# Kernel optimization log

Measured on AMD Instinct MI355X. Metric: run time of the kernel, lower is better.

The kernel has to match this reference:

```python
import jax, jax.numpy as jnp
import numpy as np

N_NODES = 20000
N_EDGES = 320000
N_GRAPHS = 64
F_IN = 128
HID = 128
K = 3
LEAK = 0.01  # nn.LeakyReLU default negative_slope


def _glorot(key, shape):
    fan_in, fan_out = shape[-2], shape[-1]
    s = jnp.sqrt(2.0 / (fan_in + fan_out))
    return jax.random.normal(key, shape, dtype=jnp.float32) * s


def setup_inputs() -> dict:
    key = jax.random.key(0)
    ks = jax.random.split(key, 12)
    x = jax.random.normal(ks[0], (N_NODES, F_IN), dtype=jnp.float32)
    edge_index = jax.random.randint(ks[1], (2, N_EDGES), 0, N_NODES, dtype=jnp.int64)
    batch = jnp.sort(jax.random.randint(ks[2], (N_NODES,), 0, N_GRAPHS, dtype=jnp.int64))
    # K-hop GraphConv weights: (K+1) matrices per layer
    W1 = _glorot(ks[3], (K + 1, F_IN, HID));       b1 = jnp.zeros((HID,), jnp.float32)
    W2 = _glorot(ks[4], (K + 1, HID, 2 * HID));    b2 = jnp.zeros((2 * HID,), jnp.float32)
    W3 = _glorot(ks[5], (K + 1, 2 * HID, 4 * HID)); b3 = jnp.zeros((4 * HID,), jnp.float32)
    # classifier MLP
    Wm1 = _glorot(ks[6], (4 * HID, 1024)); bm1 = jnp.zeros((1024,), jnp.float32)
    Wm2 = _glorot(ks[7], (1024, 512));     bm2 = jnp.zeros((512,), jnp.float32)
    Wm3 = _glorot(ks[8], (512, 4));        bm3 = jnp.zeros((4,), jnp.float32)
    return dict(x=x, edge_index=edge_index, batch=batch,
                W1=W1, b1=b1, W2=W2, b2=b2, W3=W3, b3=b3,
                Wm1=Wm1, bm1=bm1, Wm2=Wm2, bm2=bm2, Wm3=Wm3, bm3=bm3)


def _khop_conv(x, src, dst, W, b):
    # out = sum_{k=0..K} (A^k x) W_k + b, A = scatter-sum of src features onto dst
    h = x
    out = h @ W[0]
    for k in range(1, W.shape[0]):
        h = jax.ops.segment_sum(h[src], dst, num_segments=N_NODES)  # one hop
        out = out + h @ W[k]
    return out + b


def reference(x, edge_index, batch, W1, b1, W2, b2, W3, b3, Wm1, bm1, Wm2, bm2, Wm3, bm3):
    src, dst = edge_index[0], edge_index[1]
    h = _khop_conv(x, src, dst, W1, b1)
    h = jnp.where(h > 0, h, LEAK * h)
    h = _khop_conv(h, src, dst, W2, b2)
    h = jnp.where(h > 0, h, LEAK * h)
    h = _khop_conv(h, src, dst, W3, b3)
    # global max pool per graph -> [N_GRAPHS, 4*HID]
    g = jax.ops.segment_max(h, batch, num_segments=N_GRAPHS)
    # classifier head
    g = jax.nn.relu(g @ Wm1 + bm1)
    g = jax.nn.relu(g @ Wm2 + bm2)
    return g @ Wm3 + bm3
```

## Files before the change

kernel.cpp:

```cpp
#include <hip/hip_runtime.h>
#include <stdint.h>

#define NN 20000
#define NNP 20096
#define NE 320000
#define NG 64

typedef unsigned short u16;
typedef __attribute__((ext_vector_type(8))) short short8;
typedef __attribute__((ext_vector_type(4))) float f32x4;

__device__ __forceinline__ void glds16(const void* g, const void* l) {
    __builtin_amdgcn_global_load_lds((const __attribute__((address_space(1))) void*)g,
                                     (__attribute__((address_space(3))) void*)l, 16, 0, 0);
}

__device__ __forceinline__ u16 f2bf(float f) {
    unsigned u = __float_as_uint(f);
    return (u16)((u + 0x7FFFu + ((u >> 16) & 1u)) >> 16);
}

__global__ void hist_kernel(const int* __restrict__ dst, int* __restrict__ cnt, int E) {
    int i = blockIdx.x * blockDim.x + threadIdx.x;
    if (i < E) atomicAdd(&cnt[dst[i]], 1);
}

__global__ void scan_kernel(const int* __restrict__ cnt, int* __restrict__ rp, int n) {
    __shared__ int part[1024];
    int tid = threadIdx.x;
    const int CH = (n + 1023) / 1024;
    int base = tid * CH;
    int s = 0;
    for (int i = 0; i < CH; i++) { int idx = base + i; if (idx < n) s += cnt[idx]; }
    part[tid] = s;
    __syncthreads();
    for (int off = 1; off < 1024; off <<= 1) {
        int v = (tid >= off) ? part[tid - off] : 0;
        __syncthreads();
        part[tid] += v;
        __syncthreads();
    }
    int run = (tid == 0) ? 0 : part[tid - 1];
    for (int i = 0; i < CH; i++) {
        int idx = base + i;
        if (idx < n) { rp[idx] = run; run += cnt[idx]; }
    }
    if (tid == 1023) rp[n] = part[1023];
}

__global__ void copy_int(const int* __restrict__ a, int* __restrict__ b, int n) {
    int i = blockIdx.x * blockDim.x + threadIdx.x;
    if (i < n) b[i] = a[i];
}

__global__ void scatter_kernel(const int* __restrict__ src, const int* __restrict__ dstv,
                               int* __restrict__ ofs, int* __restrict__ col, int E) {
    int i = blockIdx.x * blockDim.x + threadIdx.x;
    if (i < E) {
        int p = atomicAdd(&ofs[dstv[i]], 1);
        col[p] = src[i];
    }
}

__global__ void conv_x(const float* __restrict__ x, u16* __restrict__ S1) {
    int i = blockIdx.x * blockDim.x + threadIdx.x;
    if (i >= NN * 128 / 8) return;
    int row = i >> 4, c = (i & 15) * 8;
    const float* p = x + (size_t)row * 128 + c;
    uint4 r;
    unsigned* pr = (unsigned*)&r;
#pragma unroll
    for (int j = 0; j < 4; j++)
        pr[j] = (unsigned)f2bf(p[2 * j]) | ((unsigned)f2bf(p[2 * j + 1]) << 16);
    *(uint4*)(S1 + (size_t)row * 512 + c) = r;
}

__global__ void convT(const float* __restrict__ W, u16* __restrict__ WT, int K, int M) {
    __shared__ float tile[32][33];
    int m0 = blockIdx.x * 32, k0 = blockIdx.y * 32;
    int tx = threadIdx.x & 31, ty = threadIdx.x >> 5;
#pragma unroll
    for (int i = 0; i < 32; i += 8)
        tile[ty + i][tx] = W[(size_t)(k0 + ty + i) * M + m0 + tx];
    __syncthreads();
#pragma unroll
    for (int i = 0; i < 32; i += 8)
        WT[(size_t)(m0 + ty + i) * K + k0 + tx] = f2bf(tile[tx][ty + i]);
}

__global__ void g2bf(const unsigned* __restrict__ genc, u16* __restrict__ gb) {
    int i = blockIdx.x * blockDim.x + threadIdx.x;
    if (i >= NG * 512) return;
    unsigned u = genc[i];
    u = (u & 0x80000000u) ? (u ^ 0x80000000u) : ~u;
    gb[i] = f2bf(__uint_as_float(u));
}

template <int NCHUNK>
__global__ __launch_bounds__(256) void prop_bf16(
    const int* __restrict__ rp, const int* __restrict__ col,
    u16* __restrict__ S, int stride, int in_off, int out_off) {
    constexpr int NPB = 256 / NCHUNK;
    int node = blockIdx.x * NPB + (threadIdx.x / NCHUNK);
    int c = threadIdx.x & (NCHUNK - 1);
    if (node >= NN) return;
    int s0 = rp[node], s1 = rp[node + 1];
    float acc[8] = {};
    const u16* base = S + in_off + c * 8;
    auto accum = [&](uint4 v) {
        const unsigned* pv = (const unsigned*)&v;
#pragma unroll
        for (int j = 0; j < 4; j++) {
            acc[2 * j]     += __uint_as_float(pv[j] << 16);
            acc[2 * j + 1] += __uint_as_float(pv[j] & 0xFFFF0000u);
        }
    };
    int e = s0;
    for (; e + 4 <= s1; e += 4) {
        int i0 = col[e], i1 = col[e + 1], i2 = col[e + 2], i3 = col[e + 3];
        uint4 v0 = *(const uint4*)(base + (size_t)i0 * stride);
        uint4 v1 = *(const uint4*)(base + (size_t)i1 * stride);
        uint4 v2 = *(const uint4*)(base + (size_t)i2 * stride);
        uint4 v3 = *(const uint4*)(base + (size_t)i3 * stride);
        accum(v0); accum(v1); accum(v2); accum(v3);
    }
    for (; e < s1; e++)
        accum(*(const uint4*)(base + (size_t)col[e] * stride));
    uint4 r;
    unsigned* pr = (unsigned*)&r;
#pragma unroll
    for (int j = 0; j < 4; j++)
        pr[j] = (unsigned)f2bf(acc[2 * j]) | ((unsigned)f2bf(acc[2 * j + 1]) << 16);
    *(uint4*)(S + (size_t)node * stride + out_off + c * 8) = r;
}

template <int TM, int EPI, int ACT>
__global__ __launch_bounds__(256) void gemm_bf16(
    const u16* __restrict__ A, int lda, const u16* __restrict__ BT,
    int Kp, int M, const float* __restrict__ bias,
    u16* __restrict__ outB, int ldo,
    unsigned* __restrict__ genc, const int* __restrict__ batch) {
    __shared__ u16 Al[TM * 32];
    __shared__ u16 Bl[128 * 32];
    __shared__ unsigned gbuf[EPI == 1 ? 256 : 4];
    constexpr int MR = TM / 32;
    int col0 = blockIdx.x * 128, row0 = blockIdx.y * TM;
    int t = threadIdx.x;
    int w = t >> 6, ln = t & 63;
    int wm = (w >> 1) * (TM / 2), wn = (w & 1) * 64;
    int srowB = w * 32 + (ln >> 2);
    int srowA = (TM == 128) ? srowB : (w * 16 + (ln >> 2));
    int skc = (ln & 3) * 8;
    f32x4 acc[MR][4] = {};

    if (EPI == 1) gbuf[t] = 0;

    for (int k0 = 0; k0 < Kp; k0 += 32) {
        if (TM == 128) {
            glds16(A + (size_t)(row0 + srowA) * lda + k0 + skc,      &Al[w * 1024]);
            glds16(A + (size_t)(row0 + srowA + 16) * lda + k0 + skc, &Al[w * 1024 + 512]);
        } else {
            glds16(A + (size_t)(row0 + srowA) * lda + k0 + skc,      &Al[w * 512]);
        }
        glds16(BT + (size_t)(col0 + srowB) * Kp + k0 + skc,          &Bl[w * 1024]);
        glds16(BT + (size_t)(col0 + srowB + 16) * Kp + k0 + skc,     &Bl[w * 1024 + 512]);
        __syncthreads();
        short8 af[MR], bf[4];
#pragma unroll
        for (int m = 0; m < MR; m++)
            af[m] = *(const short8*)&Al[(wm + m * 16 + (ln & 15)) * 32 + (ln >> 4) * 8];
#pragma unroll
        for (int n = 0; n < 4; n++)
            bf[n] = *(const short8*)&Bl[(wn + n * 16 + (ln & 15)) * 32 + (ln >> 4) * 8];
#pragma unroll
        for (int m = 0; m < MR; m++)
#pragma unroll
            for (int n = 0; n < 4; n++)
                acc[m][n] = __builtin_amdgcn_mfma_f32_16x16x32_bf16(af[m], bf[n], acc[m][n], 0, 0, 0);
        __syncthreads();
    }

    int g_lo = (EPI == 1) ? batch[row0] : 0;
#pragma unroll
    for (int m = 0; m < MR; m++) {
#pragma unroll
        for (int r = 0; r < 4; r++) {
            int row = row0 + wm + m * 16 + (ln >> 4) * 4 + r;
            if (row < NN) {
                int gb_ = 0, gidx = 0;
                if (EPI == 1) { gb_ = batch[row]; gidx = gb_ - g_lo; }
#pragma unroll
                for (int n = 0; n < 4; n++) {
                    int cl = wn + n * 16 + (ln & 15);
                    float v = acc[m][n][r] + bias[col0 + cl];
                    if (EPI == 0) {
                        v = ACT ? fmaxf(v, 0.f) : (v > 0.f ? v : 0.01f * v);
                        outB[(size_t)row * ldo + col0 + cl] = f2bf(v);
                    } else {
                        unsigned u = __float_as_uint(v);
                        u = (u & 0x80000000u) ? ~u : (u | 0x80000000u);
                        if (gidx < 2) atomicMax(&gbuf[gidx * 128 + cl], u);
                        else          atomicMax(&genc[(size_t)gb_ * M + col0 + cl], u);
                    }
                }
            }
        }
    }
    if (EPI == 1) {
        __syncthreads();
        int j = t >> 7, c = t & 127;
        unsigned u = gbuf[j * 128 + c];
        if (u && g_lo + j < NG) atomicMax(&genc[(size_t)(g_lo + j) * M + col0 + c], u);
    }
}

__global__ void head3(const u16* __restrict__ m2b, const float* __restrict__ W,
                      const float* __restrict__ b, float* __restrict__ outp) {
    int r = blockIdx.x;
    int w = threadIdx.x >> 6;
    int ln = threadIdx.x & 63;
    float acc = 0.f;
    for (int k = ln; k < 512; k += 64) {
        float v = __uint_as_float(((unsigned)m2b[r * 512 + k]) << 16);
        acc += v * W[k * 4 + w];
    }
#pragma unroll
    for (int o = 32; o; o >>= 1) acc += __shfl_down(acc, o, 64);
    if (ln == 0) outp[r * 4 + w] = acc + b[w];
}

extern "C" void kernel_launch(void* const* d_in, const int* in_sizes, int n_in,
                              void* d_out, int out_size, void* d_ws, size_t ws_size,
                              hipStream_t stream) {
    const float* x   = (const float*)d_in[0];
    const int*   ei  = (const int*)d_in[1];
    const int*   bat = (const int*)d_in[2];
    const float* W1  = (const float*)d_in[3];
    const float* b1  = (const float*)d_in[4];
    const float* W2  = (const float*)d_in[5];
    const float* b2  = (const float*)d_in[6];
    const float* W3  = (const float*)d_in[7];
    const float* b3  = (const float*)d_in[8];
    const float* Wm1 = (const float*)d_in[9];
    const float* bm1 = (const float*)d_in[10];
    const float* Wm2 = (const float*)d_in[11];
    const float* bm2 = (const float*)d_in[12];
    const float* Wm3 = (const float*)d_in[13];
    const float* bm3 = (const float*)d_in[14];
    float* out = (float*)d_out;

    char* ws = (char*)d_ws;
    size_t off = 0;
    auto alloc = [&](size_t bytes) -> void* {
        void* p = ws + off;
        off += (bytes + 255) & ~(size_t)255;
        return p;
    };
    int*      cnt  = (int*)alloc((size_t)NN * 4);
    int*      rp   = (int*)alloc((size_t)(NN + 1) * 4);
    int*      col  = (int*)alloc((size_t)NE * 4);
    u16*      S1   = (u16*)alloc((size_t)NNP * 512 * 2);
    u16*      S2   = (u16*)alloc((size_t)NNP * 512 * 2);
    u16*      S3   = (u16*)alloc((size_t)NNP * 1024 * 2);
    u16*      WT1  = (u16*)alloc((size_t)128 * 512 * 2);
    u16*      WT2  = (u16*)alloc((size_t)256 * 512 * 2);
    u16*      WT3  = (u16*)alloc((size_t)512 * 1024 * 2);
    u16*      WTm1 = (u16*)alloc((size_t)1024 * 512 * 2);
    u16*      WTm2 = (u16*)alloc((size_t)512 * 1024 * 2);
    unsigned* genc = (unsigned*)alloc((size_t)NG * 512 * 4);
    u16*      gb   = (u16*)alloc((size_t)NG * 512 * 2);
    u16*      m1b  = (u16*)alloc((size_t)NG * 1024 * 2);
    u16*      m2b  = (u16*)alloc((size_t)NG * 512 * 2);

    const int* src  = ei;
    const int* dstv = ei + NE;

    hipMemsetAsync(cnt, 0, (size_t)NN * 4, stream);
    hist_kernel<<<(NE + 255) / 256, 256, 0, stream>>>(dstv, cnt, NE);
    scan_kernel<<<1, 1024, 0, stream>>>(cnt, rp, NN);
    copy_int<<<(NN + 255) / 256, 256, 0, stream>>>(rp, cnt, NN);
    scatter_kernel<<<(NE + 255) / 256, 256, 0, stream>>>(src, dstv, cnt, col, NE);

    convT<<<dim3(128 / 32, 512 / 32), 256, 0, stream>>>(W1, WT1, 512, 128);
    convT<<<dim3(256 / 32, 512 / 32), 256, 0, stream>>>(W2, WT2, 512, 256);
    convT<<<dim3(512 / 32, 1024 / 32), 256, 0, stream>>>(W3, WT3, 1024, 512);
    convT<<<dim3(1024 / 32, 512 / 32), 256, 0, stream>>>(Wm1, WTm1, 512, 1024);
    convT<<<dim3(512 / 32, 1024 / 32), 256, 0, stream>>>(Wm2, WTm2, 1024, 512);

    conv_x<<<(NN * 16 + 255) / 256, 256, 0, stream>>>(x, S1);

    prop_bf16<16><<<1250, 256, 0, stream>>>(rp, col, S1, 512, 0, 128);
    prop_bf16<16><<<1250, 256, 0, stream>>>(rp, col, S1, 512, 128, 256);
    prop_bf16<16><<<1250, 256, 0, stream>>>(rp, col, S1, 512, 256, 384);
    gemm_bf16<64, 0, 0><<<dim3(1, NNP / 64), 256, 0, stream>>>(S1, 512, WT1, 512, 128, b1, S2, 512, nullptr, nullptr);

    prop_bf16<16><<<1250, 256, 0, stream>>>(rp, col, S2, 512, 0, 128);
    prop_bf16<16><<<1250, 256, 0, stream>>>(rp, col, S2, 512, 128, 256);
    prop_bf16<16><<<1250, 256, 0, stream>>>(rp, col, S2, 512, 256, 384);
    gemm_bf16<64, 0, 0><<<dim3(2, NNP / 64), 256, 0, stream>>>(S2, 512, WT2, 512, 256, b2, S3, 1024, nullptr, nullptr);

    prop_bf16<32><<<2500, 256, 0, stream>>>(rp, col, S3, 1024, 0, 256);
    prop_bf16<32><<<2500, 256, 0, stream>>>(rp, col, S3, 1024, 256, 512);
    prop_bf16<32><<<2500, 256, 0, stream>>>(rp, col, S3, 1024, 512, 768);
    hipMemsetAsync(genc, 0, (size_t)NG * 512 * 4, stream);
    gemm_bf16<128, 1, 0><<<dim3(4, NNP / 128), 256, 0, stream>>>(S3, 1024, WT3, 1024, 512, b3, nullptr, 0, genc, bat);

    g2bf<<<(NG * 512 + 255) / 256, 256, 0, stream>>>(genc, gb);
    gemm_bf16<64, 0, 1><<<dim3(8, 1), 256, 0, stream>>>(gb, 512, WTm1, 512, 1024, bm1, m1b, 1024, nullptr, nullptr);
    gemm_bf16<64, 0, 1><<<dim3(4, 1), 256, 0, stream>>>(m1b, 1024, WTm2, 1024, 512, bm2, m2b, 512, nullptr, nullptr);
    head3<<<NG, 256, 0, stream>>>(m2b, Wm3, bm3, out);
}
```

Before: 333.7 us.

## Split sparse propagation into 32-feature column windows per block

Replaces the per-node full-row gather kernel with a windowed version. Each block handles one 64-byte feature window (32 bf16) for 64 nodes, and the grid x dimension iterates over windows. The aim is to shrink the working set of each gather pass so that neighbor rows hit in L2/MALL more often. In exchange, rp and col are re-read once per window, each node's gather becomes narrower, and more blocks are launched.

Measured after the change: 345.4 us. 3.5% more time.

```diff
diff --git a/kernel.cpp b/kernel.cpp
--- a/kernel.cpp
+++ b/kernel.cpp
@@ -96,17 +96,16 @@
     gb[i] = f2bf(__uint_as_float(u));
 }
 
-template <int NCHUNK>
-__global__ __launch_bounds__(256) void prop_bf16(
+__global__ __launch_bounds__(256) void prop_win(
     const int* __restrict__ rp, const int* __restrict__ col,
     u16* __restrict__ S, int stride, int in_off, int out_off) {
-    constexpr int NPB = 256 / NCHUNK;
-    int node = blockIdx.x * NPB + (threadIdx.x / NCHUNK);
-    int c = threadIdx.x & (NCHUNK - 1);
+    int win = blockIdx.x;
+    int node = blockIdx.y * 64 + (threadIdx.x >> 2);
+    int c = (threadIdx.x & 3) * 8;
     if (node >= NN) return;
     int s0 = rp[node], s1 = rp[node + 1];
+    const u16* base = S + in_off + win * 32 + c;
     float acc[8] = {};
-    const u16* base = S + in_off + c * 8;
     auto accum = [&](uint4 v) {
         const unsigned* pv = (const unsigned*)&v;
 #pragma unroll
@@ -131,7 +130,7 @@
 #pragma unroll
     for (int j = 0; j < 4; j++)
         pr[j] = (unsigned)f2bf(acc[2 * j]) | ((unsigned)f2bf(acc[2 * j + 1]) << 16);
-    *(uint4*)(S + (size_t)node * stride + out_off + c * 8) = r;
+    *(uint4*)(S + (size_t)node * stride + out_off + win * 32 + c) = r;
 }
 
 template <int TM, int EPI, int ACT>
@@ -289,19 +288,21 @@
 
     conv_x<<<(NN * 16 + 255) / 256, 256, 0, stream>>>(x, S1);
 
-    prop_bf16<16><<<1250, 256, 0, stream>>>(rp, col, S1, 512, 0, 128);
-    prop_bf16<16><<<1250, 256, 0, stream>>>(rp, col, S1, 512, 128, 256);
-    prop_bf16<16><<<1250, 256, 0, stream>>>(rp, col, S1, 512, 256, 384);
+    const int NGY = (NN + 63) / 64;
+
+    prop_win<<<dim3(4, NGY), 256, 0, stream>>>(rp, col, S1, 512, 0, 128);
+    prop_win<<<dim3(4, NGY), 256, 0, stream>>>(rp, col, S1, 512, 128, 256);
+    prop_win<<<dim3(4, NGY), 256, 0, stream>>>(rp, col, S1, 512, 256, 384);
     gemm_bf16<64, 0, 0><<<dim3(1, NNP / 64), 256, 0, stream>>>(S1, 512, WT1, 512, 128, b1, S2, 512, nullptr, nullptr);
 
-    prop_bf16<16><<<1250, 256, 0, stream>>>(rp, col, S2, 512, 0, 128);
-    prop_bf16<16><<<1250, 256, 0, stream>>>(rp, col, S2, 512, 128, 256);
-    prop_bf16<16><<<1250, 256, 0, stream>>>(rp, col, S2, 512, 256, 384);
+    prop_win<<<dim3(4, NGY), 256, 0, stream>>>(rp, col, S2, 512, 0, 128);
+    prop_win<<<dim3(4, NGY), 256, 0, stream>>>(rp, col, S2, 512, 128, 256);
+    prop_win<<<dim3(4, NGY), 256, 0, stream>>>(rp, col, S2, 512, 256, 384);
     gemm_bf16<64, 0, 0><<<dim3(2, NNP / 64), 256, 0, stream>>>(S2, 512, WT2, 512, 256, b2, S3, 1024, nullptr, nullptr);
 
-    prop_bf16<32><<<2500, 256, 0, stream>>>(rp, col, S3, 1024, 0, 256);
-    prop_bf16<32><<<2500, 256, 0, stream>>>(rp, col, S3, 1024, 256, 512);
-    prop_bf16<32><<<2500, 256, 0, stream>>>(rp, col, S3, 1024, 512, 768);
+    prop_win<<<dim3(8, NGY), 256, 0, stream>>>(rp, col, S3, 1024, 0, 256);
+    prop_win<<<dim3(8, NGY), 256, 0, stream>>>(rp, col, S3, 1024, 256, 512);
+    prop_win<<<dim3(8, NGY), 256, 0, stream>>>(rp, col, S3, 1024, 512, 768);
     hipMemsetAsync(genc, 0, (size_t)NG * 512 * 4, stream);
     gemm_bf16<128, 1, 0><<<dim3(4, NNP / 128), 256, 0, stream>>>(S3, 1024, WT3, 1024, 512, b3, nullptr, 0, genc, bat);
 
```

## Double-buffer GEMM LDS tiles and remap blocks for XCD locality

Applied to the files above, without the earlier changes.

The bf16 MFMA GEMM now keeps two LDS buffers for the A and B tiles. It prefetches the next K-slice with global_load_lds while computing on the current one, which removes one of the two barriers per iteration. It also remaps the flat block index so that blocks land on the same XCD (eight-way round-robin) get contiguous tiles, aiming for better L2 reuse. This doubles the LDS use per block, which may lower occupancy, and it depends on the async LDS loads finishing before the next barrier.

Measured after the change: 321.8 us. 1.04x faster.

```diff
diff --git a/kernel.cpp b/kernel.cpp
--- a/kernel.cpp
+++ b/kernel.cpp
@@ -140,11 +140,17 @@
     int Kp, int M, const float* __restrict__ bias,
     u16* __restrict__ outB, int ldo,
     unsigned* __restrict__ genc, const int* __restrict__ batch) {
-    __shared__ u16 Al[TM * 32];
-    __shared__ u16 Bl[128 * 32];
+    __shared__ u16 Al[2][TM * 32];
+    __shared__ u16 Bl[2][128 * 32];
     __shared__ unsigned gbuf[EPI == 1 ? 256 : 4];
     constexpr int MR = TM / 32;
-    int col0 = blockIdx.x * 128, row0 = blockIdx.y * TM;
+    int gx = gridDim.x;
+    int total = gx * gridDim.y;
+    int flat = blockIdx.x + gx * blockIdx.y;
+    int q = total >> 3, r_ = total & 7;
+    int k8 = flat & 7, i8 = flat >> 3;
+    int v = (k8 < r_) ? (k8 * (q + 1) + i8) : (r_ * (q + 1) + (k8 - r_) * q + i8);
+    int col0 = (v % gx) * 128, row0 = (v / gx) * TM;
     int t = threadIdx.x;
     int w = t >> 6, ln = t & 63;
     int wm = (w >> 1) * (TM / 2), wn = (w & 1) * 64;
@@ -155,29 +161,35 @@
 
     if (EPI == 1) gbuf[t] = 0;
 
-    for (int k0 = 0; k0 < Kp; k0 += 32) {
-        if (TM == 128) {
-            glds16(A + (size_t)(row0 + srowA) * lda + k0 + skc,      &Al[w * 1024]);
-            glds16(A + (size_t)(row0 + srowA + 16) * lda + k0 + skc, &Al[w * 1024 + 512]);
+    auto stage = [&](int b, int k0) {
+        if constexpr (TM == 128) {
+            glds16(A + (size_t)(row0 + srowA) * lda + k0 + skc,      &Al[b][w * 1024]);
+            glds16(A + (size_t)(row0 + srowA + 16) * lda + k0 + skc, &Al[b][w * 1024 + 512]);
         } else {
-            glds16(A + (size_t)(row0 + srowA) * lda + k0 + skc,      &Al[w * 512]);
+            glds16(A + (size_t)(row0 + srowA) * lda + k0 + skc,      &Al[b][w * 512]);
         }
-        glds16(BT + (size_t)(col0 + srowB) * Kp + k0 + skc,          &Bl[w * 1024]);
-        glds16(BT + (size_t)(col0 + srowB + 16) * Kp + k0 + skc,     &Bl[w * 1024 + 512]);
+        glds16(BT + (size_t)(col0 + srowB) * Kp + k0 + skc,          &Bl[b][w * 1024]);
+        glds16(BT + (size_t)(col0 + srowB + 16) * Kp + k0 + skc,     &Bl[b][w * 1024 + 512]);
+    };
+
+    int nt = Kp / 32;
+    stage(0, 0);
+    for (int it = 0; it < nt; it++) {
+        int cur = it & 1;
         __syncthreads();
+        if (it + 1 < nt) stage(cur ^ 1, (it + 1) * 32);
         short8 af[MR], bf[4];
 #pragma unroll
         for (int m = 0; m < MR; m++)
-            af[m] = *(const short8*)&Al[(wm + m * 16 + (ln & 15)) * 32 + (ln >> 4) * 8];
+            af[m] = *(const short8*)&Al[cur][(wm + m * 16 + (ln & 15)) * 32 + (ln >> 4) * 8];
 #pragma unroll
         for (int n = 0; n < 4; n++)
-            bf[n] = *(const short8*)&Bl[(wn + n * 16 + (ln & 15)) * 32 + (ln >> 4) * 8];
+            bf[n] = *(const short8*)&Bl[cur][(wn + n * 16 + (ln & 15)) * 32 + (ln >> 4) * 8];
 #pragma unroll
         for (int m = 0; m < MR; m++)
 #pragma unroll
             for (int n = 0; n < 4; n++)
                 acc[m][n] = __builtin_amdgcn_mfma_f32_16x16x32_bf16(af[m], bf[n], acc[m][n], 0, 0, 0);
-        __syncthreads();
     }
 
     int g_lo = (EPI == 1) ? batch[row0] : 0;
@@ -192,12 +204,12 @@
 #pragma unroll
                 for (int n = 0; n < 4; n++) {
                     int cl = wn + n * 16 + (ln & 15);
-                    float v = acc[m][n][r] + bias[col0 + cl];
+                    float vv = acc[m][n][r] + bias[col0 + cl];
                     if (EPI == 0) {
-                        v = ACT ? fmaxf(v, 0.f) : (v > 0.f ? v : 0.01f * v);
-                        outB[(size_t)row * ldo + col0 + cl] = f2bf(v);
+                        vv = ACT ? fmaxf(vv, 0.f) : (vv > 0.f ? vv : 0.01f * vv);
+                        outB[(size_t)row * ldo + col0 + cl] = f2bf(vv);
                     } else {
-                        unsigned u = __float_as_uint(v);
+                        unsigned u = __float_as_uint(vv);
                         u = (u & 0x80000000u) ? ~u : (u | 0x80000000u);
                         if (gidx < 2) atomicMax(&gbuf[gidx * 128 + cl], u);
                         else          atomicMax(&genc[(size_t)gb_ * M + col0 + cl], u);
```
